# Performance work log

Hardware: AMD Instinct MI355X
Metric: run time of the kernel (lower is better)

Reference implementation:

```python
import jax, jax.numpy as jnp
import numpy as np

N_NODES = 100000
K_NEIGH = 16
C = 128
B = 1


def setup_inputs() -> dict:
    key = jax.random.key(0)
    k1, k2, k3, k4, k5, k6 = jax.random.split(key, 6)
    inp = jax.random.normal(k1, (B, C, N_NODES), dtype=jnp.float32)
    adj = jax.random.randint(k2, (N_NODES, K_NEIGH), 0, N_NODES)
    w1 = jax.random.normal(k3, (C, C), dtype=jnp.float32) * 0.05
    b1 = jax.random.normal(k4, (C,), dtype=jnp.float32) * 0.05
    w2 = jax.random.normal(k5, (C, C), dtype=jnp.float32) * 0.05
    b2 = jax.random.normal(k6, (C,), dtype=jnp.float32) * 0.05
    return {"input": inp, "adj": adj, "w1": w1, "b1": b1, "w2": w2, "b2": b2}


def reference(input, adj, w1, b1, w2, b2):
    # fc1: 1x1 conv == channel-mixing matmul. input: [B, C, N]
    state_in = jnp.einsum('oc,bcn->bon', w1, input) + b1[None, :, None]
    # gather neighbor features: [B, C, N, K], mean over neighbors -> [B, C, N]
    neigh = input[:, :, adj]            # [B, C, N, K]
    agg = neigh.mean(axis=3)            # [B, C, N]
    fwd = jnp.einsum('oc,bcn->bon', w2, agg) + b2[None, :, None]
    return state_in + fwd
```

## Files before the change

kernel.cpp:

```cpp
#include <hip/hip_runtime.h>
#include <stdint.h>

#define N_NODES 100000
#define CH 128
#define K_NEIGH 16
#define TN 32
#define XS_STRIDE 68
#define PS 132

#define PSWZ(n, o) ((n) * PS + ((o) ^ ((((n) >> 3) & 3) << 3)))


typedef short bf8v __attribute__((ext_vector_type(8)));
typedef float f32x4 __attribute__((ext_vector_type(4)));

__device__ __forceinline__ uint32_t pack_bf16x2(float a, float b) {
    union { float f; uint32_t u; } ua, ub;
    ua.f = a; ub.f = b;
    const uint32_t ra = (ua.u + 0x7fffu + ((ua.u >> 16) & 1u)) >> 16;
    const uint32_t rb = (ub.u + 0x7fffu + ((ub.u >> 16) & 1u)) >> 16;
    return ra | (rb << 16);
}
__device__ __forceinline__ uint16_t bf16_rne(float f) {
    union { float f; uint32_t u; } c; c.f = f;
    return (uint16_t)((c.u + 0x7fffu + ((c.u >> 16) & 1u)) >> 16);
}
__device__ __forceinline__ float bf16_tof(uint16_t h) {
    union { uint32_t u; float f; } c; c.u = ((uint32_t)h) << 16; return c.f;
}
__device__ __forceinline__ float bf16_lo(uint32_t u) {
    union { uint32_t u; float f; } c; c.u = u << 16; return c.f;
}
__device__ __forceinline__ float bf16_hi(uint32_t u) {
    union { uint32_t u; float f; } c; c.u = u & 0xffff0000u; return c.f;
}

__device__ __forceinline__ void cvt8(const float* __restrict__ p,
                                     bf8v& hv, bf8v& lv) {
    const float4 a = *(const float4*)p;
    const float4 b = *(const float4*)(p + 4);
    const float f[8] = {a.x, a.y, a.z, a.w, b.x, b.y, b.z, b.w};
#pragma unroll
    for (int i = 0; i < 8; ++i) {
        const uint16_t h = bf16_rne(f[i]);
        hv[i] = (short)h;
        lv[i] = (short)bf16_rne(f[i] - bf16_tof(h));
    }
}

__global__ __launch_bounds__(256, 2) void k_dual(
    const float* __restrict__ X,
    const float* __restrict__ W1,
    const float* __restrict__ W2,
    const float* __restrict__ B1,
    const float* __restrict__ B2,
    uint16_t*    __restrict__ Yt,
    float*       __restrict__ Out)
{
    __shared__ __align__(16) uint16_t XsH[64 * 128];
    __shared__ __align__(16) uint16_t XsL[64 * 128];

    const int t  = threadIdx.x;
    const int n0 = blockIdx.x * 64;
    const int V  = (N_NODES - n0 < 64) ? (N_NODES - n0) : 64;

    for (int it = 0; it < 8; ++it) {
        const int idx = t + it * 256;
        const int nq = idx & 15, c = idx >> 4;
        float4 v = make_float4(0.f, 0.f, 0.f, 0.f);
        if (nq * 4 < V)
            v = *(const float4*)&X[(size_t)c * N_NODES + n0 + nq * 4];
        const float vv0 = v.x, vv1 = v.y, vv2 = v.z, vv3 = v.w;
#pragma unroll
        for (int s = 0; s < 4; ++s) {
            const float f = (s == 0) ? vv0 : (s == 1) ? vv1 : (s == 2) ? vv2 : vv3;
            const int n = nq * 4 + s;
            const int byi = (n << 8) + (((c * 2)) ^ ((n & 7) << 4));
            const uint16_t h = bf16_rne(f);
            XsH[byi >> 1] = h;
            XsL[byi >> 1] = bf16_rne(f - bf16_tof(h));
        }
    }
    __syncthreads();

    const int l = t & 63;
    const int w = t >> 6;
    const int ar = l & 15;
    const int ac = (l >> 4) * 8;

    f32x4 d1[2][4], d2[2][4];
#pragma unroll
    for (int ot = 0; ot < 2; ++ot)
#pragma unroll
        for (int nt = 0; nt < 4; ++nt) {
            d1[ot][nt] = (f32x4){0.f, 0.f, 0.f, 0.f};
            d2[ot][nt] = (f32x4){0.f, 0.f, 0.f, 0.f};
        }

#pragma unroll
    for (int ks = 0; ks < 4; ++ks) {
        bf8v a1h[2], a1l[2], a2h[2], a2l[2];
#pragma unroll
        for (int ot = 0; ot < 2; ++ot) {
            const size_t off = (size_t)(w * 32 + ot * 16 + ar) * CH + ks * 32 + ac;
            cvt8(&W1[off], a1h[ot], a1l[ot]);
            cvt8(&W2[off], a2h[ot], a2l[ot]);
        }
#pragma unroll
        for (int nt = 0; nt < 4; ++nt) {
            const int n  = nt * 16 + (l & 15);
            const int byi = (n << 8) + ((ks * 64 + ((l >> 4) * 16)) ^ ((n & 7) << 4));
            const bf8v bh = *(const bf8v*)((const char*)XsH + byi);
            const bf8v bl = *(const bf8v*)((const char*)XsL + byi);
#pragma unroll
            for (int ot = 0; ot < 2; ++ot) {
                d1[ot][nt] = __builtin_amdgcn_mfma_f32_16x16x32_bf16(
                    a1h[ot], bh, d1[ot][nt], 0, 0, 0);
                d1[ot][nt] = __builtin_amdgcn_mfma_f32_16x16x32_bf16(
                    a1l[ot], bh, d1[ot][nt], 0, 0, 0);
                d1[ot][nt] = __builtin_amdgcn_mfma_f32_16x16x32_bf16(
                    a1h[ot], bl, d1[ot][nt], 0, 0, 0);
                d2[ot][nt] = __builtin_amdgcn_mfma_f32_16x16x32_bf16(
                    a2h[ot], bh, d2[ot][nt], 0, 0, 0);
                d2[ot][nt] = __builtin_amdgcn_mfma_f32_16x16x32_bf16(
                    a2l[ot], bh, d2[ot][nt], 0, 0, 0);
            }
        }
    }

#pragma unroll
    for (int ot = 0; ot < 2; ++ot) {
        const int ob = w * 32 + ot * 16 + (l >> 4) * 4;
        const float b0 = B1[ob + 0] + B2[ob + 0];
        const float b1 = B1[ob + 1] + B2[ob + 1];
        const float b2 = B1[ob + 2] + B2[ob + 2];
        const float b3 = B1[ob + 3] + B2[ob + 3];
#pragma unroll
        for (int nt = 0; nt < 4; ++nt) {
            const int n = nt * 16 + (l & 15);
            if (n < V) {
                float* op = Out + (size_t)ob * N_NODES + n0 + n;
                op[0]                   = d1[ot][nt][0] + b0;
                op[(size_t)N_NODES]     = d1[ot][nt][1] + b1;
                op[(size_t)N_NODES * 2] = d1[ot][nt][2] + b2;
                op[(size_t)N_NODES * 3] = d1[ot][nt][3] + b3;
            }
        }
    }

#pragma unroll
    for (int ot = 0; ot < 2; ++ot)
#pragma unroll
        for (int nt = 0; nt < 4; ++nt) {
            const int n = nt * 16 + (l & 15);
            if (n < V) {
                const int o4 = w * 32 + ot * 16 + (l >> 4) * 4;
                uint2 pv;
                pv.x = pack_bf16x2(d2[ot][nt][0], d2[ot][nt][1]);
                pv.y = pack_bf16x2(d2[ot][nt][2], d2[ot][nt][3]);
                *(uint2*)&Yt[(size_t)(n0 + n) * CH + o4] = pv;
            }
        }
}

__global__ __launch_bounds__(256, 8) void k_gather(
    const int*      __restrict__ adj,
    const uint16_t* __restrict__ Yt,
    float*          __restrict__ Out)
{
    __shared__ __align__(16) float P[TN * PS];
    __shared__ __align__(16) int adjS[TN * K_NEIGH];

    const int t  = threadIdx.x;
    const int n0 = blockIdx.x * TN;

    if (t < 128)
        *(int4*)&adjS[t * 4] = *(const int4*)&adj[(size_t)n0 * K_NEIGH + t * 4];
    __syncthreads();

    {
        const int l4 = (t & 31) * 4;
        const int g  = t >> 5;
        for (int itp = 0; itp < 4; ++itp) {
            const int n = itp * 8 + g;
            int js[K_NEIGH];
#pragma unroll
            for (int k = 0; k < K_NEIGH; ++k) js[k] = adjS[n * K_NEIGH + k];
            float4 a0 = make_float4(0.f, 0.f, 0.f, 0.f);
            float4 a1 = make_float4(0.f, 0.f, 0.f, 0.f);
#pragma unroll
            for (int k = 0; k < K_NEIGH; k += 2) {
                const uint2 v0 = *(const uint2*)&Yt[(size_t)js[k]     * CH + l4];
                const uint2 v1 = *(const uint2*)&Yt[(size_t)js[k + 1] * CH + l4];
                a0.x += bf16_lo(v0.x); a0.y += bf16_hi(v0.x);
                a0.z += bf16_lo(v0.y); a0.w += bf16_hi(v0.y);
                a1.x += bf16_lo(v1.x); a1.y += bf16_hi(v1.x);
                a1.z += bf16_lo(v1.y); a1.w += bf16_hi(v1.y);
            }
            float4 s;
            s.x = (a0.x + a1.x) * 0.0625f;
            s.y = (a0.y + a1.y) * 0.0625f;
            s.z = (a0.z + a1.z) * 0.0625f;
            s.w = (a0.w + a1.w) * 0.0625f;
            *(float4*)&P[PSWZ(n, l4)] = s;
        }
    }
    __syncthreads();

    for (int it = 0; it < 4; ++it) {
        const int idx = t + it * 256;
        const int o = idx >> 3, nq = idx & 7;
        float* op = Out + (size_t)o * N_NODES + n0 + nq * 4;
        float4 cur = *(const float4*)op;
        cur.x += P[PSWZ(nq * 4 + 0, o)];
        cur.y += P[PSWZ(nq * 4 + 1, o)];
        cur.z += P[PSWZ(nq * 4 + 2, o)];
        cur.w += P[PSWZ(nq * 4 + 3, o)];
        *(float4*)op = cur;
    }
}

__global__ __launch_bounds__(256, 2) void k_fused_legacy(
    const float* __restrict__ X,
    const int*   __restrict__ adj,
    const float* __restrict__ W1,
    const float* __restrict__ B1,
    const float* __restrict__ W2,
    const float* __restrict__ B2,
    float*       __restrict__ Out)
{
    __shared__ __align__(16) float Xs[CH * XS_STRIDE];
    __shared__ __align__(16) float As[CH * XS_STRIDE];
    __shared__ int adjS[64 * K_NEIGH];

    const int t  = threadIdx.x;
    const int n0 = blockIdx.x * 64;
    const int V  = (N_NODES - n0 < 64) ? (N_NODES - n0) : 64;

    {
        const int base  = n0 * K_NEIGH;
        const int valid = V * K_NEIGH;
        for (int idx = t; idx < 64 * K_NEIGH; idx += 256)
            adjS[idx] = (idx < valid) ? adj[base + idx] : 0;
    }
    for (int it = 0; it < 32; ++it) {
        const int idx = t + it * 256;
        const int n = idx & 63, c = idx >> 6;
        Xs[c * XS_STRIDE + n] =
            (n < V) ? X[(size_t)c * N_NODES + n0 + n] : 0.0f;
    }
    __syncthreads();

    {
        const int n_l = t & 63, q = t >> 6;
        int js[K_NEIGH];
#pragma unroll
        for (int k = 0; k < K_NEIGH; ++k) js[k] = adjS[n_l * K_NEIGH + k];
        if (n_l < V) {
            for (int cc = 0; cc < 32; ++cc) {
                const int c = q * 32 + cc;
                const float* xc = X + (size_t)c * N_NODES;
                float s = 0.0f;
#pragma unroll
                for (int k = 0; k < K_NEIGH; ++k) s += xc[js[k]];
                As[c * XS_STRIDE + n_l] = s * 0.0625f;
            }
        } else {
            for (int cc = 0; cc < 32; ++cc)
                As[(q * 32 + cc) * XS_STRIDE + n_l] = 0.0f;
        }
    }
    __syncthreads();

    const int ng = t & 7, og = t >> 3;
    float acc[4][8];
#pragma unroll
    for (int i = 0; i < 4; ++i)
#pragma unroll
        for (int j = 0; j < 8; ++j) acc[i][j] = 0.0f;

    const float* w1p = W1 + (og * 4) * CH;
    const float* w2p = W2 + (og * 4) * CH;
    for (int c = 0; c < CH; ++c) {
        float xv[8], av[8], w1v[4], w2v[4];
        *(float4*)&xv[0] = *(const float4*)&Xs[c * XS_STRIDE + ng * 8];
        *(float4*)&xv[4] = *(const float4*)&Xs[c * XS_STRIDE + ng * 8 + 4];
        *(float4*)&av[0] = *(const float4*)&As[c * XS_STRIDE + ng * 8];
        *(float4*)&av[4] = *(const float4*)&As[c * XS_STRIDE + ng * 8 + 4];
#pragma unroll
        for (int i = 0; i < 4; ++i) {
            w1v[i] = w1p[i * CH + c];
            w2v[i] = w2p[i * CH + c];
        }
#pragma unroll
        for (int i = 0; i < 4; ++i)
#pragma unroll
            for (int j = 0; j < 8; ++j)
                acc[i][j] += w1v[i] * xv[j] + w2v[i] * av[j];
    }

    __syncthreads();
    float* Zt = Xs;
#pragma unroll
    for (int i = 0; i < 4; ++i) {
        *(float4*)&Zt[(og * 4 + i) * XS_STRIDE + ng * 8]     = *(float4*)&acc[i][0];
        *(float4*)&Zt[(og * 4 + i) * XS_STRIDE + ng * 8 + 4] = *(float4*)&acc[i][4];
    }
    __syncthreads();
    for (int it = 0; it < 32; ++it) {
        const int idx = t + it * 256;
        const int n = idx & 63, o = idx >> 6;
        if (n < V) {
            Out[(size_t)o * N_NODES + n0 + n] =
                Zt[o * XS_STRIDE + n] + B1[o] + B2[o];
        }
    }
}

extern "C" void kernel_launch(void* const* d_in, const int* in_sizes, int n_in,
                              void* d_out, int out_size, void* d_ws, size_t ws_size,
                              hipStream_t stream) {
    const float* X   = (const float*)d_in[0];
    const int*   adj = (const int*)d_in[1];
    const float* W1  = (const float*)d_in[2];
    const float* B1  = (const float*)d_in[3];
    const float* W2  = (const float*)d_in[4];
    const float* B2  = (const float*)d_in[5];
    float* Out = (float*)d_out;

    const size_t yt_bytes = (size_t)N_NODES * CH * sizeof(uint16_t);

    if (ws_size >= yt_bytes) {
        uint16_t* Yt = (uint16_t*)d_ws;
        const int nb1 = (N_NODES + 63) / 64;
        k_dual<<<nb1, 256, 0, stream>>>(X, W1, W2, B1, B2, Yt, Out);
        const int nb2 = N_NODES / TN;
        k_gather<<<nb2, 256, 0, stream>>>(adj, Yt, Out);
    } else {
        const int nblocks = (N_NODES + 63) / 64;
        k_fused_legacy<<<nblocks, 256, 0, stream>>>(X, adj, W1, B1, W2, B2, Out);
    }
}
```

Baseline: 237.7 us.

## Transpose input to bf16 hi/lo node-major, then fuse gather-mean with both matmuls

The pipeline is reordered. Before, the code computed W2·X per node, gathered the projected rows, and ran a second read-modify-write pass over Out. Now a first kernel transposes X into node-major bf16 high/low split buffers, and a fused kernel gathers and averages neighbour rows of the high part, stores the aggregate as bf16 in LDS, and runs both matmuls with a single Out write. This drops the float read and rewrite of Out and the separate Yt write. In exchange, the transposed input is written twice (hi and lo), W1 and W2 are converted to bf16 in each of about 3125 blocks instead of about 1563, and the aggregate is rounded to bf16 before the W2 product.

```diff
diff --git a/kernel.cpp b/kernel.cpp
--- a/kernel.cpp
+++ b/kernel.cpp
@@ -6,9 +6,6 @@
 #define K_NEIGH 16
 #define TN 32
 #define XS_STRIDE 68
-#define PS 132
-
-#define PSWZ(n, o) ((n) * PS + ((o) ^ ((((n) >> 3) & 3) << 3)))
 
 
 typedef short bf8v __attribute__((ext_vector_type(8)));
@@ -48,17 +45,12 @@
     }
 }
 
-__global__ __launch_bounds__(256, 2) void k_dual(
+__global__ __launch_bounds__(256, 4) void k_xt(
     const float* __restrict__ X,
-    const float* __restrict__ W1,
-    const float* __restrict__ W2,
-    const float* __restrict__ B1,
-    const float* __restrict__ B2,
-    uint16_t*    __restrict__ Yt,
-    float*       __restrict__ Out)
+    uint16_t*    __restrict__ XtH,
+    uint16_t*    __restrict__ XtL)
 {
-    __shared__ __align__(16) uint16_t XsH[64 * 128];
-    __shared__ __align__(16) uint16_t XsL[64 * 128];
+    __shared__ __align__(16) float Xs[CH * XS_STRIDE];
 
     const int t  = threadIdx.x;
     const int n0 = blockIdx.x * 64;
@@ -70,15 +62,82 @@
         float4 v = make_float4(0.f, 0.f, 0.f, 0.f);
         if (nq * 4 < V)
             v = *(const float4*)&X[(size_t)c * N_NODES + n0 + nq * 4];
-        const float vv0 = v.x, vv1 = v.y, vv2 = v.z, vv3 = v.w;
-#pragma unroll
-        for (int s = 0; s < 4; ++s) {
-            const float f = (s == 0) ? vv0 : (s == 1) ? vv1 : (s == 2) ? vv2 : vv3;
-            const int n = nq * 4 + s;
-            const int byi = (n << 8) + (((c * 2)) ^ ((n & 7) << 4));
-            const uint16_t h = bf16_rne(f);
-            XsH[byi >> 1] = h;
-            XsL[byi >> 1] = bf16_rne(f - bf16_tof(h));
+        *(float4*)&Xs[c * XS_STRIDE + nq * 4] = v;
+    }
+    __syncthreads();
+
+    const int n = t & 63, half = t >> 6;
+    if (n < V) {
+        uint32_t ph[16], pl[16];
+#pragma unroll
+        for (int cc = 0; cc < 32; cc += 2) {
+            const float f0 = Xs[(half * 32 + cc) * XS_STRIDE + n];
+            const float f1 = Xs[(half * 32 + cc + 1) * XS_STRIDE + n];
+            const uint16_t h0 = bf16_rne(f0), h1 = bf16_rne(f1);
+            ph[cc >> 1] = (uint32_t)h0 | ((uint32_t)h1 << 16);
+            const uint16_t l0 = bf16_rne(f0 - bf16_tof(h0));
+            const uint16_t l1 = bf16_rne(f1 - bf16_tof(h1));
+            pl[cc >> 1] = (uint32_t)l0 | ((uint32_t)l1 << 16);
+        }
+        uint16_t* dh = &XtH[(size_t)(n0 + n) * CH + half * 32];
+        uint16_t* dl = &XtL[(size_t)(n0 + n) * CH + half * 32];
+#pragma unroll
+        for (int j = 0; j < 4; ++j) {
+            *(uint4*)&dh[j * 8] = *(uint4*)&ph[j * 4];
+            *(uint4*)&dl[j * 8] = *(uint4*)&pl[j * 4];
+        }
+    }
+}
+
+__global__ __launch_bounds__(256, 4) void k_fused2(
+    const int*      __restrict__ adj,
+    const uint16_t* __restrict__ XtH,
+    const uint16_t* __restrict__ XtL,
+    const float*    __restrict__ W1,
+    const float*    __restrict__ W2,
+    const float*    __restrict__ B1,
+    const float*    __restrict__ B2,
+    float*          __restrict__ Out)
+{
+    __shared__ __align__(16) uint16_t AggH[TN * CH];
+    __shared__ __align__(16) int adjS[TN * K_NEIGH];
+
+    const int t  = threadIdx.x;
+    const int n0 = blockIdx.x * TN;
+
+    if (t < 128)
+        *(int4*)&adjS[t * 4] = *(const int4*)&adj[(size_t)n0 * K_NEIGH + t * 4];
+    __syncthreads();
+
+    {
+        const int lq = t & 31;
+        const int l4 = lq * 4;
+        const int g  = t >> 5;
+        for (int itp = 0; itp < 4; ++itp) {
+            const int n = itp * 8 + g;
+            int js[K_NEIGH];
+#pragma unroll
+            for (int k = 0; k < K_NEIGH; ++k) js[k] = adjS[n * K_NEIGH + k];
+            float4 a0 = make_float4(0.f, 0.f, 0.f, 0.f);
+            float4 a1 = make_float4(0.f, 0.f, 0.f, 0.f);
+#pragma unroll
+            for (int k = 0; k < K_NEIGH; k += 2) {
+                const uint2 v0 = *(const uint2*)&XtH[(size_t)js[k]     * CH + l4];
+                const uint2 v1 = *(const uint2*)&XtH[(size_t)js[k + 1] * CH + l4];
+                a0.x += bf16_lo(v0.x); a0.y += bf16_hi(v0.x);
+                a0.z += bf16_lo(v0.y); a0.w += bf16_hi(v0.y);
+                a1.x += bf16_lo(v1.x); a1.y += bf16_hi(v1.x);
+                a1.z += bf16_lo(v1.y); a1.w += bf16_hi(v1.y);
+            }
+            const float sx = (a0.x + a1.x) * 0.0625f;
+            const float sy = (a0.y + a1.y) * 0.0625f;
+            const float sz = (a0.z + a1.z) * 0.0625f;
+            const float sw = (a0.w + a1.w) * 0.0625f;
+            uint2 pv;
+            pv.x = pack_bf16x2(sx, sy);
+            pv.y = pack_bf16x2(sz, sw);
+            const int byi = (n << 8) + ((8 * lq) ^ ((n & 7) << 4));
+            *(uint2*)((char*)AggH + byi) = pv;
         }
     }
     __syncthreads();
@@ -88,11 +147,11 @@
     const int ar = l & 15;
     const int ac = (l >> 4) * 8;
 
-    f32x4 d1[2][4], d2[2][4];
+    f32x4 d1[2][2], d2[2][2];
 #pragma unroll
     for (int ot = 0; ot < 2; ++ot)
 #pragma unroll
-        for (int nt = 0; nt < 4; ++nt) {
+        for (int nt = 0; nt < 2; ++nt) {
             d1[ot][nt] = (f32x4){0.f, 0.f, 0.f, 0.f};
             d2[ot][nt] = (f32x4){0.f, 0.f, 0.f, 0.f};
         }
@@ -107,11 +166,13 @@
             cvt8(&W2[off], a2h[ot], a2l[ot]);
         }
 #pragma unroll
-        for (int nt = 0; nt < 4; ++nt) {
-            const int n  = nt * 16 + (l & 15);
+        for (int nt = 0; nt < 2; ++nt) {
+            const int n = nt * 16 + (l & 15);
+            const size_t gidx = (size_t)(n0 + n) * CH + ks * 32 + ac;
+            const bf8v bh = *(const bf8v*)&XtH[gidx];
+            const bf8v bl = *(const bf8v*)&XtL[gidx];
             const int byi = (n << 8) + ((ks * 64 + ((l >> 4) * 16)) ^ ((n & 7) << 4));
-            const bf8v bh = *(const bf8v*)((const char*)XsH + byi);
-            const bf8v bl = *(const bf8v*)((const char*)XsL + byi);
+            const bf8v gh = *(const bf8v*)((const char*)AggH + byi);
 #pragma unroll
             for (int ot = 0; ot < 2; ++ot) {
                 d1[ot][nt] = __builtin_amdgcn_mfma_f32_16x16x32_bf16(
@@ -121,9 +182,9 @@
                 d1[ot][nt] = __builtin_amdgcn_mfma_f32_16x16x32_bf16(
                     a1h[ot], bl, d1[ot][nt], 0, 0, 0);
                 d2[ot][nt] = __builtin_amdgcn_mfma_f32_16x16x32_bf16(
-                    a2h[ot], bh, d2[ot][nt], 0, 0, 0);
+                    a2h[ot], gh, d2[ot][nt], 0, 0, 0);
                 d2[ot][nt] = __builtin_amdgcn_mfma_f32_16x16x32_bf16(
-                    a2l[ot], bh, d2[ot][nt], 0, 0, 0);
+                    a2l[ot], gh, d2[ot][nt], 0, 0, 0);
             }
         }
     }
@@ -136,87 +197,14 @@
         const float b2 = B1[ob + 2] + B2[ob + 2];
         const float b3 = B1[ob + 3] + B2[ob + 3];
 #pragma unroll
-        for (int nt = 0; nt < 4; ++nt) {
+        for (int nt = 0; nt < 2; ++nt) {
             const int n = nt * 16 + (l & 15);
-            if (n < V) {
-                float* op = Out + (size_t)ob * N_NODES + n0 + n;
-                op[0]                   = d1[ot][nt][0] + b0;
-                op[(size_t)N_NODES]     = d1[ot][nt][1] + b1;
-                op[(size_t)N_NODES * 2] = d1[ot][nt][2] + b2;
-                op[(size_t)N_NODES * 3] = d1[ot][nt][3] + b3;
-            }
-        }
-    }
-
-#pragma unroll
-    for (int ot = 0; ot < 2; ++ot)
-#pragma unroll
-        for (int nt = 0; nt < 4; ++nt) {
-            const int n = nt * 16 + (l & 15);
-            if (n < V) {
-                const int o4 = w * 32 + ot * 16 + (l >> 4) * 4;
-                uint2 pv;
-                pv.x = pack_bf16x2(d2[ot][nt][0], d2[ot][nt][1]);
-                pv.y = pack_bf16x2(d2[ot][nt][2], d2[ot][nt][3]);
-                *(uint2*)&Yt[(size_t)(n0 + n) * CH + o4] = pv;
-            }
-        }
-}
-
-__global__ __launch_bounds__(256, 8) void k_gather(
-    const int*      __restrict__ adj,
-    const uint16_t* __restrict__ Yt,
-    float*          __restrict__ Out)
-{
-    __shared__ __align__(16) float P[TN * PS];
-    __shared__ __align__(16) int adjS[TN * K_NEIGH];
-
-    const int t  = threadIdx.x;
-    const int n0 = blockIdx.x * TN;
-
-    if (t < 128)
-        *(int4*)&adjS[t * 4] = *(const int4*)&adj[(size_t)n0 * K_NEIGH + t * 4];
-    __syncthreads();
-
-    {
-        const int l4 = (t & 31) * 4;
-        const int g  = t >> 5;
-        for (int itp = 0; itp < 4; ++itp) {
-            const int n = itp * 8 + g;
-            int js[K_NEIGH];
-#pragma unroll
-            for (int k = 0; k < K_NEIGH; ++k) js[k] = adjS[n * K_NEIGH + k];
-            float4 a0 = make_float4(0.f, 0.f, 0.f, 0.f);
-            float4 a1 = make_float4(0.f, 0.f, 0.f, 0.f);
-#pragma unroll
-            for (int k = 0; k < K_NEIGH; k += 2) {
-                const uint2 v0 = *(const uint2*)&Yt[(size_t)js[k]     * CH + l4];
-                const uint2 v1 = *(const uint2*)&Yt[(size_t)js[k + 1] * CH + l4];
-                a0.x += bf16_lo(v0.x); a0.y += bf16_hi(v0.x);
-                a0.z += bf16_lo(v0.y); a0.w += bf16_hi(v0.y);
-                a1.x += bf16_lo(v1.x); a1.y += bf16_hi(v1.x);
-                a1.z += bf16_lo(v1.y); a1.w += bf16_hi(v1.y);
-            }
-            float4 s;
-            s.x = (a0.x + a1.x) * 0.0625f;
-            s.y = (a0.y + a1.y) * 0.0625f;
-            s.z = (a0.z + a1.z) * 0.0625f;
-            s.w = (a0.w + a1.w) * 0.0625f;
-            *(float4*)&P[PSWZ(n, l4)] = s;
-        }
-    }
-    __syncthreads();
-
-    for (int it = 0; it < 4; ++it) {
-        const int idx = t + it * 256;
-        const int o = idx >> 3, nq = idx & 7;
-        float* op = Out + (size_t)o * N_NODES + n0 + nq * 4;
-        float4 cur = *(const float4*)op;
-        cur.x += P[PSWZ(nq * 4 + 0, o)];
-        cur.y += P[PSWZ(nq * 4 + 1, o)];
-        cur.z += P[PSWZ(nq * 4 + 2, o)];
-        cur.w += P[PSWZ(nq * 4 + 3, o)];
-        *(float4*)op = cur;
+            float* op = Out + (size_t)ob * N_NODES + n0 + n;
+            op[0]                   = d1[ot][nt][0] + d2[ot][nt][0] + b0;
+            op[(size_t)N_NODES]     = d1[ot][nt][1] + d2[ot][nt][1] + b1;
+            op[(size_t)N_NODES * 2] = d1[ot][nt][2] + d2[ot][nt][2] + b2;
+            op[(size_t)N_NODES * 3] = d1[ot][nt][3] + d2[ot][nt][3] + b3;
+        }
     }
 }
 
@@ -328,14 +316,16 @@
     const float* B2  = (const float*)d_in[5];
     float* Out = (float*)d_out;
 
-    const size_t yt_bytes = (size_t)N_NODES * CH * sizeof(uint16_t);
-
-    if (ws_size >= yt_bytes) {
-        uint16_t* Yt = (uint16_t*)d_ws;
+    const size_t xt_elems = (size_t)N_NODES * CH;
+    const size_t need     = 2 * xt_elems * sizeof(uint16_t);
+
+    if (ws_size >= need) {
+        uint16_t* XtH = (uint16_t*)d_ws;
+        uint16_t* XtL = XtH + xt_elems;
         const int nb1 = (N_NODES + 63) / 64;
-        k_dual<<<nb1, 256, 0, stream>>>(X, W1, W2, B1, B2, Yt, Out);
+        k_xt<<<nb1, 256, 0, stream>>>(X, XtH, XtL);
         const int nb2 = N_NODES / TN;
-        k_gather<<<nb2, 256, 0, stream>>>(adj, Yt, Out);
+        k_fused2<<<nb2, 256, 0, stream>>>(adj, XtH, XtL, W1, W2, B1, B2, Out);
     } else {
         const int nblocks = (N_NODES + 63) / 64;
         k_fused_legacy<<<nblocks, 256, 0, stream>>>(X, adj, W1, B1, W2, B2, Out);
```

Result: faster. 229.7 us (-3.4%).
